# Kernel tuning notes

Measured on AMD Instinct MI355X. Metric: run time of the kernel, lower is better.

The kernel has to match this reference:

```python
import jax, jax.numpy as jnp
import numpy as np

EMBED_DIM = 1024
NUM_HEADS = 16
HEAD_DIM = EMBED_DIM // NUM_HEADS
BSZ, TGT, SRC = 4, 1024, 2048


def setup_inputs() -> dict:
    key = jax.random.key(0)
    ks = jax.random.split(key, 12)
    init = 1.0 / np.sqrt(EMBED_DIM)
    return {
        "hidden_states": jax.random.normal(ks[0], (BSZ, TGT, EMBED_DIM), jnp.float32),
        "key_value_states": jax.random.normal(ks[1], (BSZ, SRC, EMBED_DIM), jnp.float32),
        "bias": jax.random.normal(ks[2], (BSZ, NUM_HEADS, TGT, SRC), jnp.float32),
        "Wq": jax.random.normal(ks[3], (EMBED_DIM, EMBED_DIM), jnp.float32) * init,
        "bq": jax.random.normal(ks[4], (EMBED_DIM,), jnp.float32) * init,
        "Wk": jax.random.normal(ks[5], (EMBED_DIM, EMBED_DIM), jnp.float32) * init,
        "bk": jax.random.normal(ks[6], (EMBED_DIM,), jnp.float32) * init,
        "Wv": jax.random.normal(ks[7], (EMBED_DIM, EMBED_DIM), jnp.float32) * init,
        "bv": jax.random.normal(ks[8], (EMBED_DIM,), jnp.float32) * init,
        "Wo": jax.random.normal(ks[9], (EMBED_DIM, EMBED_DIM), jnp.float32) * init,
        "bo": jax.random.normal(ks[10], (EMBED_DIM,), jnp.float32) * init,
    }


def reference(hidden_states, key_value_states, bias, Wq, bq, Wk, bk, Wv, bv, Wo, bo):
    B, T, E = hidden_states.shape
    S = key_value_states.shape[1]
    H, hd = NUM_HEADS, HEAD_DIM
    scaling = hd ** (-0.5)
    # torch Linear: y = x @ W^T + b
    q = (hidden_states @ Wq.T + bq) * scaling            # [B,T,E]
    k = key_value_states @ Wk.T + bk                     # [B,S,E]
    v = key_value_states @ Wv.T + bv                     # [B,S,E]
    q = q.reshape(B, T, H, hd).transpose(0, 2, 1, 3)     # [B,H,T,hd]
    k = k.reshape(B, S, H, hd).transpose(0, 2, 1, 3)     # [B,H,S,hd]
    v = v.reshape(B, S, H, hd).transpose(0, 2, 1, 3)     # [B,H,S,hd]
    scores = jnp.einsum('bhtd,bhsd->bhts', q, k) + bias  # [B,H,T,S]
    probs = jax.nn.softmax(scores, axis=-1)
    attn = jnp.einsum('bhts,bhsd->bhtd', probs, v)       # [B,H,T,hd]
    # Faithful to the original: reshape (B*H, T, hd) -> (B, T, E) WITHOUT
    # transposing heads back (this is how the torch source does it).
    attn = attn.reshape(B, T, E)
    return attn @ Wo.T + bo
```

## Files before the change

### kernel.cpp

```cpp
#include <hip/hip_runtime.h>

#define DEVI __device__ __forceinline__

typedef __attribute__((ext_vector_type(4))) float f32x4;
typedef __attribute__((ext_vector_type(8))) short bf16x8;

DEVI unsigned short f2bf(float f) {
  unsigned int u = __builtin_bit_cast(unsigned int, f);
  u += 0x7FFFu + ((u >> 16) & 1u);
  return (unsigned short)(u >> 16);
}

DEVI void load_lds16(const void* g, void* l) {
  __builtin_amdgcn_global_load_lds(
      (__attribute__((address_space(1))) void*)g,
      (__attribute__((address_space(3))) void*)l,
      16, 0, 0);
}

DEVI int xcd_swz(int bid, int chunk) { return (bid & 7) * chunk + (bid >> 3); }

struct CvtArgs {
  const float* src[6];
  unsigned short* dst[6];
  int cum[6];
};

__global__ __launch_bounds__(256) void cvt_all(CvtArgs a, int total4) {
  int i = blockIdx.x * 256 + threadIdx.x;
  if (i >= total4) return;
  int s = 0;
#pragma unroll
  for (int k = 1; k < 6; ++k) s += (i >= a.cum[k]);
  const int j = i - a.cum[s];
  const f32x4 v = __builtin_nontemporal_load((const f32x4*)a.src[s] + j);
  ushort4 o;
  o.x = f2bf(v[0]); o.y = f2bf(v[1]); o.z = f2bf(v[2]); o.w = f2bf(v[3]);
  reinterpret_cast<ushort4*>(a.dst[s])[j] = o;
}

template<bool OUT_BF16>
DEVI void gemm_core(const unsigned short* __restrict__ A,
                    const unsigned short* __restrict__ W,
                    const float* __restrict__ bias,
                    void* __restrict__ out,
                    float scale, int log2R,
                    long sb, long st, long sh, long sd,
                    int bx, int by, bool vt)
{
  constexpr int K = 1024;
  __shared__ unsigned short smem[2 * 128 * 64];
  unsigned short* As = smem;
  unsigned short* Bs = smem + 8192;

  const int tid  = threadIdx.x;
  const int wid  = tid >> 6;
  const int lane = tid & 63;
  const int m0 = bx * 128;
  const int n0 = by * 128;
  const int wr = (wid >> 1) * 64;
  const int wc = (wid & 1) * 64;
  const int lg = lane >> 4;
  const int ll = lane & 15;

  f32x4 acc[4][4] = {};

  const char* Ab = (const char*)A + (long)m0 * K * 2;
  const char* Wb = (const char*)W + (long)n0 * K * 2;
  char* AsB = (char*)As;
  char* BsB = (char*)Bs;
  const long rowstride = (long)K * 2;

  for (int kt = 0; kt < K; kt += 64) {
#pragma unroll
    for (int j = 0; j < 4; ++j) {
      const int o    = (wid * 4 + j) * 1024 + lane * 16;
      const int row  = o >> 7;
      const int colb = o & 127;
      load_lds16(Ab + (long)row * rowstride + (long)kt * 2 + colb, AsB + (wid * 4 + j) * 1024);
      load_lds16(Wb + (long)row * rowstride + (long)kt * 2 + colb, BsB + (wid * 4 + j) * 1024);
    }
    __syncthreads();
#pragma unroll
    for (int ks = 0; ks < 2; ++ks) {
      bf16x8 af[4], bfr[4];
#pragma unroll
      for (int i = 0; i < 4; ++i) {
        af[i]  = *(const bf16x8*)&As[(wr + i * 16 + ll) * 64 + ks * 32 + lg * 8];
        bfr[i] = *(const bf16x8*)&Bs[(wc + i * 16 + ll) * 64 + ks * 32 + lg * 8];
      }
#pragma unroll
      for (int i = 0; i < 4; ++i)
#pragma unroll
        for (int j = 0; j < 4; ++j)
          acc[i][j] = __builtin_amdgcn_mfma_f32_16x16x32_bf16(af[i], bfr[j], acc[i][j], 0, 0, 0);
    }
    __syncthreads();
  }

  const int Rmask  = (1 << log2R) - 1;
  const int m_base = m0 + wr;
  const int b   = m_base >> log2R;
  const int tbs = m_base & Rmask;
  const int nn  = n0 + wc;
  float bj[4];
#pragma unroll
  for (int j = 0; j < 4; ++j) bj[j] = bias[nn + j * 16 + ll];

  if (OUT_BF16 && vt) {
    unsigned short* Tw = smem + wid * 2176;
#pragma unroll
    for (int h2 = 0; h2 < 2; ++h2) {
#pragma unroll
      for (int jj = 0; jj < 2; ++jj) {
        const int j = h2 * 2 + jj;
#pragma unroll
        for (int i = 0; i < 4; ++i)
#pragma unroll
          for (int r = 0; r < 4; ++r)
            Tw[(jj * 16 + ll) * 68 + i * 16 + lg * 4 + r] = f2bf((acc[i][j][r] + bj[j]) * scale);
      }
      asm volatile("s_waitcnt lgkmcnt(0)" ::: "memory");
#pragma unroll
      for (int k = 0; k < 8; ++k) {
        const int dloc = k * 4 + lg;
        const int t4   = ll * 4;
        const ushort4 vv = *(const ushort4*)&Tw[dloc * 68 + t4];
        const int n = nn + h2 * 32 + dloc;
        const int h = n >> 6, dd = n & 63;
        *(ushort4*)((unsigned short*)out + (long)b * sb + (long)h * sh + (long)dd * sd + tbs + t4) = vv;
      }
      if (h2 == 0) asm volatile("s_waitcnt lgkmcnt(0)" ::: "memory");
    }
    return;
  }

  if (OUT_BF16) {
    const int h = nn >> 6;
    unsigned short* ob = (unsigned short*)out + (long)b * sb + (long)h * sh;
    unsigned short* Tw = smem + wid * 2176;
#pragma unroll
    for (int p = 0; p < 2; ++p) {
#pragma unroll
      for (int i2 = 0; i2 < 2; ++i2) {
        const int i = p * 2 + i2;
#pragma unroll
        for (int j = 0; j < 4; ++j)
#pragma unroll
          for (int r = 0; r < 4; ++r)
            Tw[(i2 * 16 + lg * 4 + r) * 68 + j * 16 + ll] = f2bf((acc[i][j][r] + bj[j]) * scale);
      }
      asm volatile("s_waitcnt lgkmcnt(0)" ::: "memory");
#pragma unroll
      for (int k = 0; k < 8; ++k) {
        const int t_loc = k * 4 + lg;
        const int d4    = ll * 4;
        const ushort4 vv = *(const ushort4*)&Tw[t_loc * 68 + d4];
        *(ushort4*)(ob + (long)(tbs + p * 32 + t_loc) * st + d4) = vv;
      }
      if (p == 0) asm volatile("s_waitcnt lgkmcnt(0)" ::: "memory");
    }
    return;
  }

  {
    float* ob = (float*)out + (long)b * sb + nn;
    float* TwF = (float*)smem + wid * 1056;
#pragma unroll
    for (int i = 0; i < 4; ++i) {
#pragma unroll
      for (int j = 0; j < 4; ++j)
#pragma unroll
        for (int r = 0; r < 4; ++r)
          TwF[(lg * 4 + r) * 66 + j * 16 + ll] = acc[i][j][r] + bj[j];
      asm volatile("s_waitcnt lgkmcnt(0)" ::: "memory");
#pragma unroll
      for (int k = 0; k < 8; ++k) {
        const int t_loc = k * 2 + (lane >> 5);
        const int c2    = (lane & 31) * 2;
        const float2 v = *(const float2*)&TwF[t_loc * 66 + c2];
        *(float2*)(ob + (long)(tbs + i * 16 + t_loc) * st + c2) = v;
      }
      if (i < 3) asm volatile("s_waitcnt lgkmcnt(0)" ::: "memory");
    }
  }
}

struct GemmDesc {
  const unsigned short* A;
  const unsigned short* W;
  const float* bias;
  unsigned short* out;
  float scale;
  int log2R;
  long sb, st, sh, sd;
};

__global__ __launch_bounds__(256) void gemm_qkv(GemmDesc d0, GemmDesc d1, GemmDesc d2) {
  int bid = xcd_swz(blockIdx.x, 160);
  const GemmDesc* d;
  bool vt = false;
  if (bid < 256)      { d = &d0; }
  else if (bid < 768) { d = &d1; bid -= 256; }
  else                { d = &d2; bid -= 768; vt = true; }
  gemm_core<true>(d->A, d->W, d->bias, d->out, d->scale, d->log2R,
                  d->sb, d->st, d->sh, d->sd, bid >> 3, bid & 7, vt);
}

__global__ __launch_bounds__(256) void gemm_o(
    const unsigned short* __restrict__ A,
    const unsigned short* __restrict__ W,
    const float* __restrict__ bias,
    float* __restrict__ out,
    long sb, long st, long sh, long sd)
{
  const int bid = xcd_swz(blockIdx.x, 32);
  gemm_core<false>(A, W, bias, out, 1.0f, 10, sb, st, sh, sd, bid >> 3, bid & 7, false);
}

__global__ __launch_bounds__(512, 4) void attn_fused(
    const unsigned short* __restrict__ Qb,
    const unsigned short* __restrict__ Kb,
    const unsigned short* __restrict__ Vt,
    const float* __restrict__ bias,
    unsigned short* __restrict__ Ob)
{
  constexpr int T = 1024, S = 2048, NC = S / 64;
  __shared__ unsigned short Ks[64 * 72];
  __shared__ unsigned short Vs[64 * 72];
  __shared__ unsigned short Ps[8][16 * 72];

  const int tid = threadIdx.x;
  const int w = tid >> 6, lane = tid & 63;
  const int lg = lane >> 4, ll = lane & 15;

  const int wg = xcd_swz(blockIdx.x, 64);
  const int bh = wg >> 3;
  const int tt = wg & 7;
  const int trow = tt * 128 + w * 16;

  bf16x8 qf[2];
#pragma unroll
  for (int ks = 0; ks < 2; ++ks)
    qf[ks] = *(const bf16x8*)(Qb + ((long)bh * T + trow + ll) * 64 + ks * 32 + lg * 8);

  f32x4 acc[4] = {};
  float m_run = -1e30f, l_run = 0.0f;

  const char* Kg = (const char*)(Kb + (long)bh * S * 64);
  const char* Vg = (const char*)(Vt + (long)bh * 64 * S);
  const float* bias_row = bias + ((long)bh * T + trow + ll) * S + lg * 4;
  unsigned short* Pw = &Ps[w][0];

  const int srow = tid >> 3;
  const int scolb = (tid & 7) * 16;

  for (int sc = 0; sc < NC; ++sc) {
    const float* bp = bias_row + sc * 64;
    f32x4 b4[4];
#pragma unroll
    for (int sf = 0; sf < 4; ++sf)
      b4[sf] = __builtin_nontemporal_load((const f32x4*)(bp + sf * 16));

    {
      const uint4 kd = *(const uint4*)(Kg + (long)(sc * 64 + srow) * 128 + scolb);
      *(uint4*)((char*)&Ks[0] + srow * 144 + scolb) = kd;
      const uint4 vd = *(const uint4*)(Vg + (long)srow * (S * 2) + sc * 128 + scolb);
      *(uint4*)((char*)&Vs[0] + srow * 144 + scolb) = vd;
    }
    __syncthreads();

    f32x4 sv[4] = {};
    __builtin_amdgcn_s_setprio(1);
#pragma unroll
    for (int ks = 0; ks < 2; ++ks) {
      bf16x8 kf[4];
#pragma unroll
      for (int sf = 0; sf < 4; ++sf)
        kf[sf] = *(const bf16x8*)((const char*)&Ks[0] + (sf * 16 + ll) * 144 + (ks * 32 + lg * 8) * 2);
#pragma unroll
      for (int sf = 0; sf < 4; ++sf)
        sv[sf] = __builtin_amdgcn_mfma_f32_16x16x32_bf16(kf[sf], qf[ks], sv[sf], 0, 0, 0);
    }
    __builtin_amdgcn_s_setprio(0);

#pragma unroll
    for (int sf = 0; sf < 4; ++sf) {
      sv[sf][0] += b4[sf][0]; sv[sf][1] += b4[sf][1];
      sv[sf][2] += b4[sf][2]; sv[sf][3] += b4[sf][3];
    }

    float cm = sv[0][0];
#pragma unroll
    for (int sf = 0; sf < 4; ++sf)
#pragma unroll
      for (int r = 0; r < 4; ++r) cm = fmaxf(cm, sv[sf][r]);
    cm = fmaxf(cm, __shfl_xor(cm, 16));
    cm = fmaxf(cm, __shfl_xor(cm, 32));

    const float mnew = fmaxf(m_run, cm);
    const float alpha = __expf(m_run - mnew);
    float ps = 0.0f;
#pragma unroll
    for (int sf = 0; sf < 4; ++sf)
#pragma unroll
      for (int r = 0; r < 4; ++r) {
        const float p = __expf(sv[sf][r] - mnew);
        sv[sf][r] = p;
        ps += p;
      }
    ps += __shfl_xor(ps, 16);
    ps += __shfl_xor(ps, 32);
    l_run = l_run * alpha + ps;
    m_run = mnew;

    float ar[4];
#pragma unroll
    for (int r = 0; r < 4; ++r) ar[r] = __shfl(alpha, lg * 4 + r);
#pragma unroll
    for (int df = 0; df < 4; ++df)
#pragma unroll
      for (int r = 0; r < 4; ++r) acc[df][r] *= ar[r];

#pragma unroll
    for (int sf = 0; sf < 4; ++sf) {
      ushort4 pw;
      pw.x = f2bf(sv[sf][0]); pw.y = f2bf(sv[sf][1]);
      pw.z = f2bf(sv[sf][2]); pw.w = f2bf(sv[sf][3]);
      *(ushort4*)&Pw[ll * 72 + sf * 16 + lg * 4] = pw;
    }
    asm volatile("s_waitcnt lgkmcnt(0)" ::: "memory");
    __builtin_amdgcn_sched_barrier(0);

    __builtin_amdgcn_s_setprio(1);
#pragma unroll
    for (int ks = 0; ks < 2; ++ks) {
      bf16x8 pa = *(const bf16x8*)((const char*)Pw + ll * 144 + ks * 64 + lg * 16);
      bf16x8 vf[4];
#pragma unroll
      for (int df = 0; df < 4; ++df)
        vf[df] = *(const bf16x8*)((const char*)&Vs[0] + (df * 16 + ll) * 144 + (ks * 32 + lg * 8) * 2);
#pragma unroll
      for (int df = 0; df < 4; ++df)
        acc[df] = __builtin_amdgcn_mfma_f32_16x16x32_bf16(pa, vf[df], acc[df], 0, 0, 0);
    }
    __builtin_amdgcn_s_setprio(0);
    __syncthreads();
  }

  const float inv = 1.0f / l_run;
  float ir[4];
#pragma unroll
  for (int r = 0; r < 4; ++r) ir[r] = __shfl(inv, lg * 4 + r);
#pragma unroll
  for (int df = 0; df < 4; ++df)
#pragma unroll
    for (int r = 0; r < 4; ++r) {
      const long oo = ((long)bh * T + trow + lg * 4 + r) * 64 + df * 16 + ll;
      Ob[oo] = f2bf(acc[df][r] * ir[r]);
    }
}

extern "C" void kernel_launch(void* const* d_in, const int* in_sizes, int n_in,
                              void* d_out, int out_size, void* d_ws, size_t ws_size,
                              hipStream_t stream) {
  constexpr int B = 4, T = 1024, S = 2048, E = 1024;
  const float* hs   = (const float*)d_in[0];
  const float* kv   = (const float*)d_in[1];
  const float* bias = (const float*)d_in[2];
  const float* Wq   = (const float*)d_in[3];
  const float* bq   = (const float*)d_in[4];
  const float* Wk   = (const float*)d_in[5];
  const float* bk   = (const float*)d_in[6];
  const float* Wv   = (const float*)d_in[7];
  const float* bv   = (const float*)d_in[8];
  const float* Wo   = (const float*)d_in[9];
  const float* bo   = (const float*)d_in[10];

  char* ws = (char*)d_ws;
  const size_t MB = 1024 * 1024;
  unsigned short* hs_bf = (unsigned short*)(ws);
  unsigned short* kv_bf = (unsigned short*)(ws + 8 * MB);
  unsigned short* wq_bf = (unsigned short*)(ws + 24 * MB);
  unsigned short* wk_bf = (unsigned short*)(ws + 26 * MB);
  unsigned short* wv_bf = (unsigned short*)(ws + 28 * MB);
  unsigned short* wo_bf = (unsigned short*)(ws + 30 * MB);
  unsigned short* q_buf = (unsigned short*)(ws + 32 * MB);
  unsigned short* k_buf = (unsigned short*)(ws + 40 * MB);
  unsigned short* v_buf = (unsigned short*)(ws + 56 * MB);
  unsigned short* a_buf = (unsigned short*)(ws + 72 * MB);

  CvtArgs ca;
  ca.src[0] = hs;  ca.dst[0] = hs_bf;
  ca.src[1] = kv;  ca.dst[1] = kv_bf;
  ca.src[2] = Wq;  ca.dst[2] = wq_bf;
  ca.src[3] = Wk;  ca.dst[3] = wk_bf;
  ca.src[4] = Wv;  ca.dst[4] = wv_bf;
  ca.src[5] = Wo;  ca.dst[5] = wo_bf;
  const int n4_hs = B * T * E / 4, n4_kv = B * S * E / 4, n4_w = E * E / 4;
  ca.cum[0] = 0;
  ca.cum[1] = n4_hs;
  ca.cum[2] = n4_hs + n4_kv;
  ca.cum[3] = n4_hs + n4_kv + n4_w;
  ca.cum[4] = n4_hs + n4_kv + 2 * n4_w;
  ca.cum[5] = n4_hs + n4_kv + 3 * n4_w;
  const int total4 = n4_hs + n4_kv + 4 * n4_w;
  cvt_all<<<dim3((total4 + 255) / 256), dim3(256), 0, stream>>>(ca, total4);

  GemmDesc dq{hs_bf, wq_bf, bq, q_buf, 0.125f, 10,
              (long)T * E, 64L, (long)T * 64, 1L};
  GemmDesc dk{kv_bf, wk_bf, bk, k_buf, 1.0f, 11,
              (long)S * E, 64L, (long)S * 64, 1L};
  GemmDesc dv{kv_bf, wv_bf, bv, v_buf, 1.0f, 11,
              (long)S * E, 1L, (long)S * 64, (long)S};
  gemm_qkv<<<dim3(1280), 256, 0, stream>>>(dq, dk, dv);

  attn_fused<<<dim3(512), dim3(512), 0, stream>>>(q_buf, k_buf, v_buf, bias, a_buf);

  gemm_o<<<dim3(256), 256, 0, stream>>>(
      a_buf, wo_bf, bo, (float*)d_out,
      (long)T * E, (long)E, 64L, 1L);
}
```

Baseline: 273.2 us.

## Double-buffer K/V tiles in attention via async global-to-LDS loads with XOR swizzle

Replaces the synchronous register-staged K/V tile copy with direct global_load_lds into a double-buffered LDS, prefetching the next chunk while the current one is computed. The padded 72-stride layout becomes a dense 64-stride layout with XOR swizzle to avoid bank conflicts, and reads are adjusted to match. Synchronization uses a manual vmcnt wait plus raw s_barrier, so the ordering relative to the bias loads is tuned by hand and could race if the vmcnt count is wrong. LDS use grows with the second buffer, which may affect occupancy.

```diff
diff --git a/kernel.cpp b/kernel.cpp
--- a/kernel.cpp
+++ b/kernel.cpp
@@ -226,8 +226,8 @@
     unsigned short* __restrict__ Ob)
 {
   constexpr int T = 1024, S = 2048, NC = S / 64;
-  __shared__ unsigned short Ks[64 * 72];
-  __shared__ unsigned short Vs[64 * 72];
+  __shared__ unsigned short Ks[2][64 * 64];
+  __shared__ unsigned short Vs[2][64 * 64];
   __shared__ unsigned short Ps[8][16 * 72];
 
   const int tid = threadIdx.x;
@@ -253,34 +253,48 @@
   unsigned short* Pw = &Ps[w][0];
 
   const int srow = tid >> 3;
-  const int scolb = (tid & 7) * 16;
+  const int scb  = ((tid & 7) * 16) ^ ((srow & 7) << 4);
+  char* ksW = (char*)&Ks[0][0] + w * 1024;
+  char* vsW = (char*)&Vs[0][0] + w * 1024;
+
+  auto stageK = [&](int sc, int buf) {
+    load_lds16(Kg + (long)(sc * 64 + srow) * 128 + scb, ksW + buf * 8192);
+  };
+  auto stageV = [&](int sc, int buf) {
+    load_lds16(Vg + (long)srow * (S * 2) + sc * 128 + scb, vsW + buf * 8192);
+  };
+
+  stageK(0, 0);
+  stageV(0, 0);
 
   for (int sc = 0; sc < NC; ++sc) {
+    const int cur = sc & 1;
+    const int nsc = (sc + 1 < NC) ? sc + 1 : 0;
+    stageK(nsc, cur ^ 1);
+    stageV(nsc, cur ^ 1);
+
     const float* bp = bias_row + sc * 64;
     f32x4 b4[4];
 #pragma unroll
     for (int sf = 0; sf < 4; ++sf)
       b4[sf] = __builtin_nontemporal_load((const f32x4*)(bp + sf * 16));
 
-    {
-      const uint4 kd = *(const uint4*)(Kg + (long)(sc * 64 + srow) * 128 + scolb);
-      *(uint4*)((char*)&Ks[0] + srow * 144 + scolb) = kd;
-      const uint4 vd = *(const uint4*)(Vg + (long)srow * (S * 2) + sc * 128 + scolb);
-      *(uint4*)((char*)&Vs[0] + srow * 144 + scolb) = vd;
-    }
-    __syncthreads();
+    __builtin_amdgcn_sched_barrier(0);
+    asm volatile("s_waitcnt vmcnt(6)" ::: "memory");
+    __builtin_amdgcn_s_barrier();
+    __builtin_amdgcn_sched_barrier(0);
 
     f32x4 sv[4] = {};
     __builtin_amdgcn_s_setprio(1);
 #pragma unroll
     for (int ks = 0; ks < 2; ++ks) {
-      bf16x8 kf[4];
-#pragma unroll
-      for (int sf = 0; sf < 4; ++sf)
-        kf[sf] = *(const bf16x8*)((const char*)&Ks[0] + (sf * 16 + ll) * 144 + (ks * 32 + lg * 8) * 2);
-#pragma unroll
-      for (int sf = 0; sf < 4; ++sf)
-        sv[sf] = __builtin_amdgcn_mfma_f32_16x16x32_bf16(kf[sf], qf[ks], sv[sf], 0, 0, 0);
+#pragma unroll
+      for (int sf = 0; sf < 4; ++sf) {
+        const int r = sf * 16 + ll;
+        const int c = (ks * 64 + lg * 16) ^ ((r & 7) << 4);
+        const bf16x8 kf = *(const bf16x8*)((const char*)&Ks[cur][0] + r * 128 + c);
+        sv[sf] = __builtin_amdgcn_mfma_f32_16x16x32_bf16(kf, qf[ks], sv[sf], 0, 0, 0);
+      }
     }
     __builtin_amdgcn_s_setprio(0);
 
@@ -336,16 +350,19 @@
 #pragma unroll
     for (int ks = 0; ks < 2; ++ks) {
       bf16x8 pa = *(const bf16x8*)((const char*)Pw + ll * 144 + ks * 64 + lg * 16);
-      bf16x8 vf[4];
-#pragma unroll
-      for (int df = 0; df < 4; ++df)
-        vf[df] = *(const bf16x8*)((const char*)&Vs[0] + (df * 16 + ll) * 144 + (ks * 32 + lg * 8) * 2);
-#pragma unroll
-      for (int df = 0; df < 4; ++df)
-        acc[df] = __builtin_amdgcn_mfma_f32_16x16x32_bf16(pa, vf[df], acc[df], 0, 0, 0);
+#pragma unroll
+      for (int df = 0; df < 4; ++df) {
+        const int d = df * 16 + ll;
+        const int c = (ks * 64 + lg * 16) ^ ((d & 7) << 4);
+        const bf16x8 vf = *(const bf16x8*)((const char*)&Vs[cur][0] + d * 128 + c);
+        acc[df] = __builtin_amdgcn_mfma_f32_16x16x32_bf16(pa, vf, acc[df], 0, 0, 0);
+      }
     }
     __builtin_amdgcn_s_setprio(0);
-    __syncthreads();
+
+    __builtin_amdgcn_sched_barrier(0);
+    __builtin_amdgcn_s_barrier();
+    __builtin_amdgcn_sched_barrier(0);
   }
 
   const float inv = 1.0f / l_run;
```

Measured after the change: 273.6 us. No clear change (+0.2%).

## Double-buffer GEMM K-tiles with smaller 32-wide K steps

Applied to the files above, without the earlier changes.

The projection GEMM main loop now splits K into 32-wide tiles held in two LDS buffers. The global-to-LDS load for the next tile is issued before the MFMAs on the current tile, so each iteration needs one barrier instead of two. The intent is to overlap global memory latency with compute. In exchange each barrier covers half as much MFMA work, there is more loop overhead per unit of K, and LDS reads now use a 64-byte row stride that may cause bank conflicts.

```diff
diff --git a/kernel.cpp b/kernel.cpp
--- a/kernel.cpp
+++ b/kernel.cpp
@@ -48,10 +48,8 @@
                     long sb, long st, long sh, long sd,
                     int bx, int by, bool vt)
 {
-  constexpr int K = 1024;
-  __shared__ unsigned short smem[2 * 128 * 64];
-  unsigned short* As = smem;
-  unsigned short* Bs = smem + 8192;
+  constexpr int K = 1024, NT = K / 32;
+  __shared__ unsigned short smem[2 * 8192];
 
   const int tid  = threadIdx.x;
   const int wid  = tid >> 6;
@@ -67,34 +65,44 @@
 
   const char* Ab = (const char*)A + (long)m0 * K * 2;
   const char* Wb = (const char*)W + (long)n0 * K * 2;
-  char* AsB = (char*)As;
-  char* BsB = (char*)Bs;
   const long rowstride = (long)K * 2;
 
-  for (int kt = 0; kt < K; kt += 64) {
-#pragma unroll
-    for (int j = 0; j < 4; ++j) {
-      const int o    = (wid * 4 + j) * 1024 + lane * 16;
-      const int row  = o >> 7;
-      const int colb = o & 127;
-      load_lds16(Ab + (long)row * rowstride + (long)kt * 2 + colb, AsB + (wid * 4 + j) * 1024);
-      load_lds16(Wb + (long)row * rowstride + (long)kt * 2 + colb, BsB + (wid * 4 + j) * 1024);
-    }
-    __syncthreads();
-#pragma unroll
-    for (int ks = 0; ks < 2; ++ks) {
-      bf16x8 af[4], bfr[4];
-#pragma unroll
-      for (int i = 0; i < 4; ++i) {
-        af[i]  = *(const bf16x8*)&As[(wr + i * 16 + ll) * 64 + ks * 32 + lg * 8];
-        bfr[i] = *(const bf16x8*)&Bs[(wc + i * 16 + ll) * 64 + ks * 32 + lg * 8];
-      }
-#pragma unroll
-      for (int i = 0; i < 4; ++i)
-#pragma unroll
-        for (int j = 0; j < 4; ++j)
-          acc[i][j] = __builtin_amdgcn_mfma_f32_16x16x32_bf16(af[i], bfr[j], acc[i][j], 0, 0, 0);
-    }
+  const int r_off = lane >> 2;
+  const int cb    = (lane & 3) * 16;
+
+  auto stage = [&](int tile, int buf) {
+    const long ktb = (long)tile * 64;
+    char* base = (char*)smem + buf * 16384;
+#pragma unroll
+    for (int c = 0; c < 2; ++c) {
+      const int ch  = 2 * wid + c;
+      const int row = ch * 16 + r_off;
+      load_lds16(Ab + (long)row * rowstride + ktb + cb, base + ch * 1024);
+      load_lds16(Wb + (long)row * rowstride + ktb + cb, base + 8192 + ch * 1024);
+    }
+  };
+
+  auto compute = [&](int buf) {
+    const char* base = (const char*)smem + buf * 16384;
+    bf16x8 af[4], bfr[4];
+#pragma unroll
+    for (int i = 0; i < 4; ++i) {
+      af[i]  = *(const bf16x8*)(base + (wr + i * 16 + ll) * 64 + lg * 16);
+      bfr[i] = *(const bf16x8*)(base + 8192 + (wc + i * 16 + ll) * 64 + lg * 16);
+    }
+#pragma unroll
+    for (int i = 0; i < 4; ++i)
+#pragma unroll
+      for (int j = 0; j < 4; ++j)
+        acc[i][j] = __builtin_amdgcn_mfma_f32_16x16x32_bf16(af[i], bfr[j], acc[i][j], 0, 0, 0);
+  };
+
+  stage(0, 0);
+  __syncthreads();
+  for (int kt = 0; kt < NT; ++kt) {
+    const int cur = kt & 1;
+    if (kt + 1 < NT) stage(kt + 1, cur ^ 1);
+    compute(cur);
     __syncthreads();
   }
 
```

New measurement: 254.6 us. 6.8% less time.
